# Performance work log

Measured on AMD Instinct MI355X. Metric: run time of the kernel, lower is better.

Reference implementation:

```python
import jax, jax.numpy as jnp
import numpy as np

RANK = 32
W0 = 30.0


def lip_linear(x, w, c, b=None):
    # LipschitzLinear: scale rows of w so row-wise L1 norm <= softplus(c)
    scale = jnp.minimum(jax.nn.softplus(c) / jnp.sum(jnp.abs(w), axis=-1), 1.0)
    y = x @ (w * scale[:, None]).T
    return y + b if b is not None else y


def setup_inputs() -> dict:
    key = jax.random.key(0)
    ks = jax.random.split(key, 20)
    d = {}
    d['coords'] = jax.random.normal(ks[0], (8, 32768, 3), dtype=jnp.float32)
    d['latents'] = jax.random.normal(ks[1], (8, 128), dtype=jnp.float32)
    d['nf_w_first'] = jax.random.normal(ks[2], (256, 3), dtype=jnp.float32)
    d['nf_b_first'] = jax.random.normal(ks[3], (256,), dtype=jnp.float32)
    d['nf_c_first'] = jax.random.uniform(ks[4], (1,), dtype=jnp.float32)
    d['nf_w_hid'] = jax.random.normal(ks[5], (3, 256, 256), dtype=jnp.float32)
    d['nf_b_hid'] = jax.random.normal(ks[6], (3, 256), dtype=jnp.float32)
    d['nf_c_hid'] = jax.random.uniform(ks[7], (3,), dtype=jnp.float32)
    d['nf_w_last'] = jax.random.normal(ks[8], (1, 256), dtype=jnp.float32)
    d['nf_b_last'] = jax.random.normal(ks[9], (1,), dtype=jnp.float32)
    d['nf_c_last'] = jax.random.uniform(ks[10], (1,), dtype=jnp.float32)
    d['Aw_first'] = jax.random.normal(ks[11], (96, 128), dtype=jnp.float32)
    d['Ac_first'] = jax.random.uniform(ks[12], (1,), dtype=jnp.float32)
    d['Aw_hid'] = jax.random.normal(ks[13], (3, 8192, 128), dtype=jnp.float32)
    d['Ac_hid'] = jax.random.uniform(ks[14], (3,), dtype=jnp.float32)
    d['Bw'] = jax.random.normal(ks[15], (4, 8192, 128), dtype=jnp.float32)
    d['Bc'] = jax.random.uniform(ks[16], (4,), dtype=jnp.float32)
    d['hbw'] = jax.random.normal(ks[17], (4, 256, 128), dtype=jnp.float32)
    d['hbc'] = jax.random.uniform(ks[18], (4,), dtype=jnp.float32)
    return d


def reference(coords, latents, nf_w_first, nf_b_first, nf_c_first, nf_w_hid, nf_b_hid, nf_c_hid,
              nf_w_last, nf_b_last, nf_c_last, Aw_first, Ac_first, Aw_hid, Ac_hid, Bw, Bc, hbw, hbc):
    T = latents.shape[0]
    # assemble per-layer params: (nf_w, nf_b, nf_c, A_w, A_c, B_w, B_c, hb_w, hb_c)
    layers = [(nf_w_first, nf_b_first, nf_c_first, Aw_first, Ac_first, Bw[0], Bc[0], hbw[0], hbc[0])]
    for j in range(nf_w_hid.shape[0]):
        layers.append((nf_w_hid[j], nf_b_hid[j], nf_c_hid[j], Aw_hid[j], Ac_hid[j],
                       Bw[j + 1], Bc[j + 1], hbw[j + 1], hbc[j + 1]))

    x = coords  # [T, N, d_in]
    for (w, b, c, aw, ac, bw, bc, hw, hc) in layers:
        d_out, d_in = w.shape
        A = lip_linear(latents, aw, ac).reshape(T, d_in, RANK)   # [T, d_in, r]
        B = lip_linear(latents, bw, bc).reshape(T, RANK, d_out)  # [T, r, d_out]
        bias = lip_linear(latents, hw, hc)                       # [T, d_out]
        base = lip_linear(x, w, c, b)                            # [T, N, d_out]
        mod = jnp.einsum('tnr,tro->tno', jnp.einsum('tni,tir->tnr', x, A), B)
        x = jnp.sin(W0 * (base + mod + bias[:, None, :]))
    return lip_linear(x, nf_w_last, nf_c_last, nf_b_last)  # [T, N, 1]
```

## Files before the change

kernel.cpp:

```cpp
#include <hip/hip_runtime.h>
#include <math.h>

#define W0F 30.0f
#define NPTS 32768

#define C_30_OVER_2PI 4.774648292756860070
#define C_2PI         6.283185307179586477

typedef double v4d __attribute__((ext_vector_type(4)));

#define OFF_M    0ull
#define SZ_M     2097152ull
#define OFF_CB   (OFF_M + SZ_M)
#define SZ_CB    8192ull
#define OFF_AF   (OFF_CB + SZ_CB)
#define SZ_AF    262144ull
#define OFF_BF   (OFF_AF + SZ_AF)
#define SZ_BF    262144ull
#define OFF_HB   (OFF_BF + SZ_BF)
#define SZ_HB    8192ull
#define OFF_NSC  (OFF_HB + SZ_HB)
#define SZ_NSC   2048ull
#define OFF_X    (OFF_NSC + SZ_NSC)
#define SZ_X     16777216ull

__global__ __launch_bounds__(256) void setup1(
    const float* __restrict__ latents,
    const float* __restrict__ AwF, const float* __restrict__ AcF,
    const float* __restrict__ AwH, const float* __restrict__ AcH,
    const float* __restrict__ Bw,  const float* __restrict__ Bc,
    const float* __restrict__ hbw, const float* __restrict__ hbc,
    const float* __restrict__ wF,  const float* __restrict__ cF,
    const float* __restrict__ wH,  const float* __restrict__ cH,
    const float* __restrict__ wL,  const float* __restrict__ cL,
    float* __restrict__ AF, float* __restrict__ BFo,
    float* __restrict__ HBo, float* __restrict__ NSC)
{
    __shared__ float lat[1024];
    int tid = threadIdx.x;
    for (int j = tid; j < 1024; j += 256) lat[j] = latents[j];
    __syncthreads();
    int g = blockIdx.x * 256 + tid;
    if (g < 58464) {
        const float* src; float c; float* dst; int stride;
        if (g < 96) {
            src = AwF + g * 128; c = AcF[0]; dst = AF + g; stride = 8192;
        } else if (g < 24672) {
            int q = g - 96; int l = 1 + q / 8192;
            src = AwH + (size_t)q * 128; c = AcH[l - 1];
            dst = AF + (size_t)l * 8 * 8192 + (q % 8192); stride = 8192;
        } else if (g < 57440) {
            int q = g - 24672; int l = q / 8192;
            src = Bw + (size_t)q * 128; c = Bc[l];
            dst = BFo + (size_t)l * 8 * 8192 + (q % 8192); stride = 8192;
        } else {
            int q = g - 57440; int l = q / 256;
            src = hbw + (size_t)q * 128; c = hbc[l];
            dst = HBo + l * 8 * 256 + (q % 256); stride = 256;
        }
        double l1 = 0.0;
        double acc[8] = {0,0,0,0,0,0,0,0};
        for (int kk = 0; kk < 32; ++kk) {
            float4 w4 = ((const float4*)src)[kk];
            l1 += fabs((double)w4.x) + fabs((double)w4.y)
                + fabs((double)w4.z) + fabs((double)w4.w);
            int k = kk * 4;
            #pragma unroll
            for (int t = 0; t < 8; ++t) {
                const float* lp = &lat[t * 128 + k];
                acc[t] = fma((double)w4.x, (double)lp[0], acc[t]);
                acc[t] = fma((double)w4.y, (double)lp[1], acc[t]);
                acc[t] = fma((double)w4.z, (double)lp[2], acc[t]);
                acc[t] = fma((double)w4.w, (double)lp[3], acc[t]);
            }
        }
        double s = fmin(log1p(exp((double)c)) / l1, 1.0);
        #pragma unroll
        for (int t = 0; t < 8; ++t) dst[(size_t)t * stride] = (float)(acc[t] * s);
    } else if (g < 59489) {
        int h = g - 58464;
        if (h < 256) {
            const float* src = wF + h * 3;
            double l1 = fabs((double)src[0]) + fabs((double)src[1]) + fabs((double)src[2]);
            NSC[h] = (float)fmin(log1p(exp((double)cF[0])) / l1, 1.0);
        } else if (h < 1024) {
            int q = h - 256; int l = 1 + q / 256;
            const float* src = wH + (size_t)q * 256;
            double l1 = 0.0;
            for (int kk = 0; kk < 64; ++kk) {
                float4 w4 = ((const float4*)src)[kk];
                l1 += fabs((double)w4.x) + fabs((double)w4.y)
                    + fabs((double)w4.z) + fabs((double)w4.w);
            }
            NSC[256 + q] = (float)fmin(log1p(exp((double)cH[l - 1])) / l1, 1.0);
        } else {
            double l1 = 0.0;
            for (int kk = 0; kk < 64; ++kk) {
                float4 w4 = ((const float4*)wL)[kk];
                l1 += fabs((double)w4.x) + fabs((double)w4.y)
                    + fabs((double)w4.z) + fabs((double)w4.w);
            }
            NSC[1024] = (float)fmin(log1p(exp((double)cL[0])) / l1, 1.0);
        }
    }
}

__global__ __launch_bounds__(256) void setup2(
    const float* __restrict__ wF, const float* __restrict__ bF,
    const float* __restrict__ wH, const float* __restrict__ bH,
    const float* __restrict__ AF, const float* __restrict__ BFi,
    const float* __restrict__ HBi, const float* __restrict__ NSC,
    float* __restrict__ Mb, float* __restrict__ CBb)
{
    int b = blockIdx.x; int t = b / 49; int rem = b % 49;
    int o = threadIdx.x;
    int l, i0, ni;
    if (rem == 0) { l = 0; i0 = 0; ni = 3; }
    else { l = 1 + (rem - 1) / 16; i0 = ((rem - 1) % 16) * 16; ni = 16; }
    size_t ltb = (size_t)(l * 8 + t);
    const float* af = AF + ltb * 8192;
    const float* bf = BFi + ltb * 8192;
    double sc = (double)NSC[l * 256 + o];
    float bcol[32];
    #pragma unroll
    for (int r = 0; r < 32; ++r) bcol[r] = bf[r * 256 + o];
    for (int ii = 0; ii < ni; ++ii) {
        int i = i0 + ii;
        float wv = (l == 0) ? wF[o * 3 + i] : wH[(size_t)((l - 1) * 256 + o) * 256 + i];
        double m = (double)wv * sc;
        #pragma unroll
        for (int r = 0; r < 32; ++r)
            m = fma((double)af[i * 32 + r], (double)bcol[r], m);
        Mb[ltb * 65536 + (size_t)i * 256 + o] = (float)m;
    }
    if (rem == 0 || ((rem - 1) % 16) == 0) {
        double bb = (l == 0) ? (double)bF[o] : (double)bH[(l - 1) * 256 + o];
        CBb[ltb * 256 + o] = (float)(bb + (double)HBi[ltb * 256 + o]);
    }
}

__device__ __forceinline__ float sin30(double z) {
    double u = z * C_30_OVER_2PI;
    double r = u - rint(u);
    return sinf((float)(r * C_2PI));
}

__global__ __launch_bounds__(256) void layer0_k(
    const float* __restrict__ coords, const float* __restrict__ Mb,
    const float* __restrict__ CBb, float* __restrict__ X, int tbase)
{
    __shared__ float Ms[3][256];
    __shared__ float cbs[256];
    int tid = threadIdx.x;
    int tl = blockIdx.x >> 10; int rb = blockIdx.x & 1023;
    int t = tbase + tl;
    const float* Mt = Mb + (size_t)t * 65536;
    Ms[0][tid] = Mt[tid]; Ms[1][tid] = Mt[256 + tid]; Ms[2][tid] = Mt[512 + tid];
    cbs[tid] = CBb[t * 256 + tid];
    __syncthreads();
    int r = rb * 32 + (tid >> 3); int lane8 = tid & 7;
    const float* cp = coords + ((size_t)t * NPTS + r) * 3;
    double c0 = (double)cp[0], c1 = (double)cp[1], c2 = (double)cp[2];
    float* xo = X + ((size_t)tl * NPTS + r) * 256;
#define L0E(col) sin30(fma(c2, (double)Ms[2][col], fma(c1, (double)Ms[1][col], \
                  fma(c0, (double)Ms[0][col], (double)cbs[col]))))
    #pragma unroll
    for (int j = 0; j < 8; ++j) {
        int col = 4 * lane8 + 32 * j;
        float4 v;
        v.x = L0E(col + 0);
        v.y = L0E(col + 1);
        v.z = L0E(col + 2);
        v.w = L0E(col + 3);
        *(float4*)(xo + col) = v;
    }
#undef L0E
}

__global__ __launch_bounds__(256, 2) void gemm_sin(
    float* __restrict__ X, const float* __restrict__ Mb,
    const float* __restrict__ CBb, int l, int tbase)
{
    __shared__ float As[16][72];
    __shared__ float Bs[16][264];
    __shared__ float cbs[256];
    int tid = threadIdx.x;
    int tl = blockIdx.x >> 9; int rb = blockIdx.x & 511;
    size_t ltb = (size_t)(l * 8 + tbase + tl);
    const float* Mt = Mb + ltb * 65536;
    float* Xt = X + ((size_t)tl * NPTS + rb * 64) * 256;
    cbs[tid] = CBb[ltb * 256 + tid];
    int wave = tid >> 6, lane = tid & 63;
    int q = lane >> 4, c16 = lane & 15;
    v4d zz = {0., 0., 0., 0.};
    v4d p1 = __builtin_amdgcn_mfma_f64_16x16x4f64((double)(1 << c16), 1.0, zz, 0, 0, 0);
    v4d p2 = __builtin_amdgcn_mfma_f64_16x16x4f64(1.0, (double)(1 << c16), zz, 0, 0, 0);
    int r0 = 61 - __builtin_clzll((unsigned long long)p1[0]);
    int r1 = 61 - __builtin_clzll((unsigned long long)p1[1]);
    int r2 = 61 - __builtin_clzll((unsigned long long)p1[2]);
    int r3 = 61 - __builtin_clzll((unsigned long long)p1[3]);
    int c0 = 61 - __builtin_clzll((unsigned long long)p2[0]);
    int c1 = 61 - __builtin_clzll((unsigned long long)p2[1]);
    int c2 = 61 - __builtin_clzll((unsigned long long)p2[2]);
    int c3 = 61 - __builtin_clzll((unsigned long long)p2[3]);
    int arow = tid >> 2;
    int ak4  = (tid & 3) * 4;
    int bch  = tid & 63;
    int br0  = tid >> 6;
    v4d acc0 = {0.,0.,0.,0.}, acc1 = {0.,0.,0.,0.}, acc2 = {0.,0.,0.,0.},
        acc3 = {0.,0.,0.,0.}, acc4 = {0.,0.,0.,0.}, acc5 = {0.,0.,0.,0.},
        acc6 = {0.,0.,0.,0.}, acc7 = {0.,0.,0.,0.}, acc8 = {0.,0.,0.,0.},
        acc9 = {0.,0.,0.,0.}, acc10 = {0.,0.,0.,0.}, acc11 = {0.,0.,0.,0.},
        acc12 = {0.,0.,0.,0.}, acc13 = {0.,0.,0.,0.}, acc14 = {0.,0.,0.,0.},
        acc15 = {0.,0.,0.,0.};
    for (int kb = 0; kb < 16; ++kb) {
        float4 a0 = *(const float4*)(Xt + (size_t)arow * 256 + kb * 16 + ak4);
        const float* Bg = Mt + (size_t)kb * 16 * 256 + bch * 4;
        float4 b0 = *(const float4*)(Bg + (br0 +  0) * 256);
        float4 b1 = *(const float4*)(Bg + (br0 +  4) * 256);
        float4 b2 = *(const float4*)(Bg + (br0 +  8) * 256);
        float4 b3 = *(const float4*)(Bg + (br0 + 12) * 256);
        __syncthreads();
        As[ak4+0][arow] = a0.x; As[ak4+1][arow] = a0.y;
        As[ak4+2][arow] = a0.z; As[ak4+3][arow] = a0.w;
        *(float4*)&Bs[br0 +  0][bch * 4] = b0;
        *(float4*)&Bs[br0 +  4][bch * 4] = b1;
        *(float4*)&Bs[br0 +  8][bch * 4] = b2;
        *(float4*)&Bs[br0 + 12][bch * 4] = b3;
        __syncthreads();
        #pragma unroll
        for (int k4 = 0; k4 < 4; ++k4) {
            int kk = k4 * 4 + q;
            double av = (double)As[kk][wave * 16 + c16];
#define TILE(n) { double bv = (double)Bs[kk][(n) * 16 + c16];                  \
                  acc##n = __builtin_amdgcn_mfma_f64_16x16x4f64(              \
                               av, bv, acc##n, 0, 0, 0); }
            TILE(0)  TILE(1)  TILE(2)  TILE(3)
            TILE(4)  TILE(5)  TILE(6)  TILE(7)
            TILE(8)  TILE(9)  TILE(10) TILE(11)
            TILE(12) TILE(13) TILE(14) TILE(15)
#undef TILE
        }
    }
    float* Xw = Xt + (size_t)(wave * 16) * 256;
#define EPT(n) {                                                               \
        int cb0 = (n) * 16;                                                    \
        Xw[r0 * 256 + cb0 + c0] = sin30(acc##n[0] + (double)cbs[cb0 + c0]);    \
        Xw[r1 * 256 + cb0 + c1] = sin30(acc##n[1] + (double)cbs[cb0 + c1]);    \
        Xw[r2 * 256 + cb0 + c2] = sin30(acc##n[2] + (double)cbs[cb0 + c2]);    \
        Xw[r3 * 256 + cb0 + c3] = sin30(acc##n[3] + (double)cbs[cb0 + c3]); }
    EPT(0)  EPT(1)  EPT(2)  EPT(3)
    EPT(4)  EPT(5)  EPT(6)  EPT(7)
    EPT(8)  EPT(9)  EPT(10) EPT(11)
    EPT(12) EPT(13) EPT(14) EPT(15)
#undef EPT
}

__global__ __launch_bounds__(256) void final_k(
    const float* __restrict__ X, const float* __restrict__ wl,
    const float* __restrict__ bl, const float* __restrict__ NSC,
    float* __restrict__ out, int tbase)
{
    int tid = threadIdx.x; int w = tid >> 6; int lane = tid & 63;
    size_t row = (size_t)blockIdx.x * 4 + w;
    double ls = (double)NSC[1024];
    float4 wv = ((const float4*)wl)[lane];
    float4 xv = *(const float4*)(X + row * 256 + lane * 4);
    double d = 0.0;
    d = fma((double)wv.x, (double)xv.x, d);
    d = fma((double)wv.y, (double)xv.y, d);
    d = fma((double)wv.z, (double)xv.z, d);
    d = fma((double)wv.w, (double)xv.w, d);
    d *= ls;
    #pragma unroll
    for (int off = 32; off > 0; off >>= 1) d += __shfl_down(d, off, 64);
    if (lane == 0) out[(size_t)tbase * NPTS + row] = (float)(d + (double)bl[0]);
}

extern "C" void kernel_launch(void* const* d_in, const int* in_sizes, int n_in,
                              void* d_out, int out_size, void* d_ws, size_t ws_size,
                              hipStream_t stream)
{
    const float* coords     = (const float*)d_in[0];
    const float* latents    = (const float*)d_in[1];
    const float* nf_w_first = (const float*)d_in[2];
    const float* nf_b_first = (const float*)d_in[3];
    const float* nf_c_first = (const float*)d_in[4];
    const float* nf_w_hid   = (const float*)d_in[5];
    const float* nf_b_hid   = (const float*)d_in[6];
    const float* nf_c_hid   = (const float*)d_in[7];
    const float* nf_w_last  = (const float*)d_in[8];
    const float* nf_b_last  = (const float*)d_in[9];
    const float* nf_c_last  = (const float*)d_in[10];
    const float* Aw_first   = (const float*)d_in[11];
    const float* Ac_first   = (const float*)d_in[12];
    const float* Aw_hid     = (const float*)d_in[13];
    const float* Ac_hid     = (const float*)d_in[14];
    const float* Bw         = (const float*)d_in[15];
    const float* Bc         = (const float*)d_in[16];
    const float* hbw        = (const float*)d_in[17];
    const float* hbc        = (const float*)d_in[18];

    float* ws  = (float*)d_ws;
    float* Mb  = ws + OFF_M;
    float* CBb = ws + OFF_CB;
    float* AF  = ws + OFF_AF;
    float* BFb = ws + OFF_BF;
    float* HBb = ws + OFF_HB;
    float* NSC = ws + OFF_NSC;
    float* X   = ws + OFF_X;
    float* out = (float*)d_out;

    setup1<<<233, 256, 0, stream>>>(latents, Aw_first, Ac_first, Aw_hid, Ac_hid,
                                    Bw, Bc, hbw, hbc,
                                    nf_w_first, nf_c_first, nf_w_hid, nf_c_hid,
                                    nf_w_last, nf_c_last,
                                    AF, BFb, HBb, NSC);
    setup2<<<392, 256, 0, stream>>>(nf_w_first, nf_b_first, nf_w_hid, nf_b_hid,
                                    AF, BFb, HBb, NSC, Mb, CBb);
    for (int tbase = 0; tbase < 8; tbase += 2) {
        layer0_k<<<2048, 256, 0, stream>>>(coords, Mb, CBb, X, tbase);
        for (int l = 1; l <= 3; ++l)
            gemm_sin<<<1024, 256, 0, stream>>>(X, Mb, CBb, l, tbase);
        final_k<<<16384, 256, 0, stream>>>(X, nf_w_last, nf_b_last, NSC, out, tbase);
    }
}
```

Before: 2.328 ms.

## Double-buffer shared-memory tiles in gemm_sin and raise occupancy hint

Splits the A and B shared-memory tiles into two buffers. Global loads for the next k-block are issued before the MFMA work on the current block, so load latency can overlap with compute and each iteration needs one barrier instead of two. Launch bounds move from 2 to 3 blocks per SM, which limits registers per thread. With 64 fp64 accumulator values plus the prefetch registers this risks spilling, and double buffering doubles LDS use.

```diff
diff --git a/kernel.cpp b/kernel.cpp
--- a/kernel.cpp
+++ b/kernel.cpp
@@ -177,12 +177,12 @@
 #undef L0E
 }
 
-__global__ __launch_bounds__(256, 2) void gemm_sin(
+__global__ __launch_bounds__(256, 3) void gemm_sin(
     float* __restrict__ X, const float* __restrict__ Mb,
     const float* __restrict__ CBb, int l, int tbase)
 {
-    __shared__ float As[16][72];
-    __shared__ float Bs[16][264];
+    __shared__ float As[2][16][72];
+    __shared__ float Bs[2][16][264];
     __shared__ float cbs[256];
     int tid = threadIdx.x;
     int tl = blockIdx.x >> 9; int rb = blockIdx.x & 511;
@@ -213,26 +213,38 @@
         acc9 = {0.,0.,0.,0.}, acc10 = {0.,0.,0.,0.}, acc11 = {0.,0.,0.,0.},
         acc12 = {0.,0.,0.,0.}, acc13 = {0.,0.,0.,0.}, acc14 = {0.,0.,0.,0.},
         acc15 = {0.,0.,0.,0.};
-    for (int kb = 0; kb < 16; ++kb) {
-        float4 a0 = *(const float4*)(Xt + (size_t)arow * 256 + kb * 16 + ak4);
-        const float* Bg = Mt + (size_t)kb * 16 * 256 + bch * 4;
+    {
+        float4 a0 = *(const float4*)(Xt + (size_t)arow * 256 + ak4);
+        const float* Bg = Mt + bch * 4;
         float4 b0 = *(const float4*)(Bg + (br0 +  0) * 256);
         float4 b1 = *(const float4*)(Bg + (br0 +  4) * 256);
         float4 b2 = *(const float4*)(Bg + (br0 +  8) * 256);
         float4 b3 = *(const float4*)(Bg + (br0 + 12) * 256);
-        __syncthreads();
-        As[ak4+0][arow] = a0.x; As[ak4+1][arow] = a0.y;
-        As[ak4+2][arow] = a0.z; As[ak4+3][arow] = a0.w;
-        *(float4*)&Bs[br0 +  0][bch * 4] = b0;
-        *(float4*)&Bs[br0 +  4][bch * 4] = b1;
-        *(float4*)&Bs[br0 +  8][bch * 4] = b2;
-        *(float4*)&Bs[br0 + 12][bch * 4] = b3;
-        __syncthreads();
+        As[0][ak4+0][arow] = a0.x; As[0][ak4+1][arow] = a0.y;
+        As[0][ak4+2][arow] = a0.z; As[0][ak4+3][arow] = a0.w;
+        *(float4*)&Bs[0][br0 +  0][bch * 4] = b0;
+        *(float4*)&Bs[0][br0 +  4][bch * 4] = b1;
+        *(float4*)&Bs[0][br0 +  8][bch * 4] = b2;
+        *(float4*)&Bs[0][br0 + 12][bch * 4] = b3;
+    }
+    __syncthreads();
+    #pragma unroll 2
+    for (int kb = 0; kb < 16; ++kb) {
+        int cur = kb & 1, nxt = cur ^ 1;
+        float4 a0, b0, b1, b2, b3;
+        if (kb < 15) {
+            a0 = *(const float4*)(Xt + (size_t)arow * 256 + (kb + 1) * 16 + ak4);
+            const float* Bg = Mt + (size_t)(kb + 1) * 16 * 256 + bch * 4;
+            b0 = *(const float4*)(Bg + (br0 +  0) * 256);
+            b1 = *(const float4*)(Bg + (br0 +  4) * 256);
+            b2 = *(const float4*)(Bg + (br0 +  8) * 256);
+            b3 = *(const float4*)(Bg + (br0 + 12) * 256);
+        }
         #pragma unroll
         for (int k4 = 0; k4 < 4; ++k4) {
             int kk = k4 * 4 + q;
-            double av = (double)As[kk][wave * 16 + c16];
-#define TILE(n) { double bv = (double)Bs[kk][(n) * 16 + c16];                  \
+            double av = (double)As[cur][kk][wave * 16 + c16];
+#define TILE(n) { double bv = (double)Bs[cur][kk][(n) * 16 + c16];             \
                   acc##n = __builtin_amdgcn_mfma_f64_16x16x4f64(              \
                                av, bv, acc##n, 0, 0, 0); }
             TILE(0)  TILE(1)  TILE(2)  TILE(3)
@@ -241,6 +253,15 @@
             TILE(12) TILE(13) TILE(14) TILE(15)
 #undef TILE
         }
+        if (kb < 15) {
+            As[nxt][ak4+0][arow] = a0.x; As[nxt][ak4+1][arow] = a0.y;
+            As[nxt][ak4+2][arow] = a0.z; As[nxt][ak4+3][arow] = a0.w;
+            *(float4*)&Bs[nxt][br0 +  0][bch * 4] = b0;
+            *(float4*)&Bs[nxt][br0 +  4][bch * 4] = b1;
+            *(float4*)&Bs[nxt][br0 +  8][bch * 4] = b2;
+            *(float4*)&Bs[nxt][br0 + 12][bch * 4] = b3;
+        }
+        __syncthreads();
     }
     float* Xw = Xt + (size_t)(wave * 16) * 256;
 #define EPT(n) {                                                               \
```

After: 2.186 ms. 1.07x faster.

## Split gemm_sin columns across blocks, read operands directly, ping-pong X buffers

Applied to the files above, without the earlier changes.

Each gemm_sin block now computes half of the 256 output columns for 64 rows, which doubles the grid and halves the accumulator count so that occupancy can rise to 4 blocks per SM. The LDS staging and the per-k-block __syncthreads are removed, and each lane loads its A and B scalars straight from global memory through the cache. Because two blocks now read the same rows in place, the layers ping-pong between two X buffers. This drops barrier and LDS overhead but issues many more uncoalesced scalar global loads and reads the A rows twice.

```diff
diff --git a/kernel.cpp b/kernel.cpp
--- a/kernel.cpp
+++ b/kernel.cpp
@@ -21,8 +21,9 @@
 #define SZ_HB    8192ull
 #define OFF_NSC  (OFF_HB + SZ_HB)
 #define SZ_NSC   2048ull
-#define OFF_X    (OFF_NSC + SZ_NSC)
+#define OFF_X0   (OFF_NSC + SZ_NSC)
 #define SZ_X     16777216ull
+#define OFF_X1   (OFF_X0 + SZ_X)
 
 __global__ __launch_bounds__(256) void setup1(
     const float* __restrict__ latents,
@@ -177,19 +178,21 @@
 #undef L0E
 }
 
-__global__ __launch_bounds__(256, 2) void gemm_sin(
-    float* __restrict__ X, const float* __restrict__ Mb,
-    const float* __restrict__ CBb, int l, int tbase)
-{
-    __shared__ float As[16][72];
-    __shared__ float Bs[16][264];
-    __shared__ float cbs[256];
+__global__ __launch_bounds__(256, 4) void gemm_sin(
+    const float* __restrict__ Xsrc, float* __restrict__ Xdst,
+    const float* __restrict__ Mb, const float* __restrict__ CBb,
+    int l, int tbase)
+{
     int tid = threadIdx.x;
-    int tl = blockIdx.x >> 9; int rb = blockIdx.x & 511;
+    int b = blockIdx.x;
+    int tl = b >> 10;
+    int rb = (b >> 1) & 511;
+    int ch = b & 1;
     size_t ltb = (size_t)(l * 8 + tbase + tl);
-    const float* Mt = Mb + ltb * 65536;
-    float* Xt = X + ((size_t)tl * NPTS + rb * 64) * 256;
-    cbs[tid] = CBb[ltb * 256 + tid];
+    const float* Mt  = Mb + ltb * 65536 + ch * 128;
+    const float* cbp = CBb + ltb * 256 + ch * 128;
+    const float* Xs = Xsrc + ((size_t)tl * NPTS + rb * 64) * 256;
+    float*       Xd = Xdst + ((size_t)tl * NPTS + rb * 64) * 256 + ch * 128;
     int wave = tid >> 6, lane = tid & 63;
     int q = lane >> 4, c16 = lane & 15;
     v4d zz = {0., 0., 0., 0.};
@@ -203,56 +206,31 @@
     int c1 = 61 - __builtin_clzll((unsigned long long)p2[1]);
     int c2 = 61 - __builtin_clzll((unsigned long long)p2[2]);
     int c3 = 61 - __builtin_clzll((unsigned long long)p2[3]);
-    int arow = tid >> 2;
-    int ak4  = (tid & 3) * 4;
-    int bch  = tid & 63;
-    int br0  = tid >> 6;
+    const float* ap = Xs + (size_t)(wave * 16 + c16) * 256 + q;
+    const float* bp = Mt + (size_t)q * 256 + c16;
     v4d acc0 = {0.,0.,0.,0.}, acc1 = {0.,0.,0.,0.}, acc2 = {0.,0.,0.,0.},
         acc3 = {0.,0.,0.,0.}, acc4 = {0.,0.,0.,0.}, acc5 = {0.,0.,0.,0.},
-        acc6 = {0.,0.,0.,0.}, acc7 = {0.,0.,0.,0.}, acc8 = {0.,0.,0.,0.},
-        acc9 = {0.,0.,0.,0.}, acc10 = {0.,0.,0.,0.}, acc11 = {0.,0.,0.,0.},
-        acc12 = {0.,0.,0.,0.}, acc13 = {0.,0.,0.,0.}, acc14 = {0.,0.,0.,0.},
-        acc15 = {0.,0.,0.,0.};
-    for (int kb = 0; kb < 16; ++kb) {
-        float4 a0 = *(const float4*)(Xt + (size_t)arow * 256 + kb * 16 + ak4);
-        const float* Bg = Mt + (size_t)kb * 16 * 256 + bch * 4;
-        float4 b0 = *(const float4*)(Bg + (br0 +  0) * 256);
-        float4 b1 = *(const float4*)(Bg + (br0 +  4) * 256);
-        float4 b2 = *(const float4*)(Bg + (br0 +  8) * 256);
-        float4 b3 = *(const float4*)(Bg + (br0 + 12) * 256);
-        __syncthreads();
-        As[ak4+0][arow] = a0.x; As[ak4+1][arow] = a0.y;
-        As[ak4+2][arow] = a0.z; As[ak4+3][arow] = a0.w;
-        *(float4*)&Bs[br0 +  0][bch * 4] = b0;
-        *(float4*)&Bs[br0 +  4][bch * 4] = b1;
-        *(float4*)&Bs[br0 +  8][bch * 4] = b2;
-        *(float4*)&Bs[br0 + 12][bch * 4] = b3;
-        __syncthreads();
-        #pragma unroll
-        for (int k4 = 0; k4 < 4; ++k4) {
-            int kk = k4 * 4 + q;
-            double av = (double)As[kk][wave * 16 + c16];
-#define TILE(n) { double bv = (double)Bs[kk][(n) * 16 + c16];                  \
+        acc6 = {0.,0.,0.,0.}, acc7 = {0.,0.,0.,0.};
+    #pragma unroll 4
+    for (int s = 0; s < 64; ++s) {
+        double av = (double)ap[4 * s];
+        const float* bb = bp + (size_t)s * 1024;
+#define TILE(n) { double bv = (double)bb[(n) * 16];                            \
                   acc##n = __builtin_amdgcn_mfma_f64_16x16x4f64(              \
                                av, bv, acc##n, 0, 0, 0); }
-            TILE(0)  TILE(1)  TILE(2)  TILE(3)
-            TILE(4)  TILE(5)  TILE(6)  TILE(7)
-            TILE(8)  TILE(9)  TILE(10) TILE(11)
-            TILE(12) TILE(13) TILE(14) TILE(15)
+        TILE(0) TILE(1) TILE(2) TILE(3)
+        TILE(4) TILE(5) TILE(6) TILE(7)
 #undef TILE
-        }
-    }
-    float* Xw = Xt + (size_t)(wave * 16) * 256;
+    }
+    float* Xw = Xd + (size_t)(wave * 16) * 256;
 #define EPT(n) {                                                               \
         int cb0 = (n) * 16;                                                    \
-        Xw[r0 * 256 + cb0 + c0] = sin30(acc##n[0] + (double)cbs[cb0 + c0]);    \
-        Xw[r1 * 256 + cb0 + c1] = sin30(acc##n[1] + (double)cbs[cb0 + c1]);    \
-        Xw[r2 * 256 + cb0 + c2] = sin30(acc##n[2] + (double)cbs[cb0 + c2]);    \
-        Xw[r3 * 256 + cb0 + c3] = sin30(acc##n[3] + (double)cbs[cb0 + c3]); }
-    EPT(0)  EPT(1)  EPT(2)  EPT(3)
-    EPT(4)  EPT(5)  EPT(6)  EPT(7)
-    EPT(8)  EPT(9)  EPT(10) EPT(11)
-    EPT(12) EPT(13) EPT(14) EPT(15)
+        Xw[r0 * 256 + cb0 + c0] = sin30(acc##n[0] + (double)cbp[cb0 + c0]);    \
+        Xw[r1 * 256 + cb0 + c1] = sin30(acc##n[1] + (double)cbp[cb0 + c1]);    \
+        Xw[r2 * 256 + cb0 + c2] = sin30(acc##n[2] + (double)cbp[cb0 + c2]);    \
+        Xw[r3 * 256 + cb0 + c3] = sin30(acc##n[3] + (double)cbp[cb0 + c3]); }
+    EPT(0) EPT(1) EPT(2) EPT(3)
+    EPT(4) EPT(5) EPT(6) EPT(7)
 #undef EPT
 }
 
@@ -308,7 +286,8 @@
     float* BFb = ws + OFF_BF;
     float* HBb = ws + OFF_HB;
     float* NSC = ws + OFF_NSC;
-    float* X   = ws + OFF_X;
+    float* X0  = ws + OFF_X0;
+    float* X1  = ws + OFF_X1;
     float* out = (float*)d_out;
 
     setup1<<<233, 256, 0, stream>>>(latents, Aw_first, Ac_first, Aw_hid, Ac_hid,
@@ -319,9 +298,10 @@
     setup2<<<392, 256, 0, stream>>>(nf_w_first, nf_b_first, nf_w_hid, nf_b_hid,
                                     AF, BFb, HBb, NSC, Mb, CBb);
     for (int tbase = 0; tbase < 8; tbase += 2) {
-        layer0_k<<<2048, 256, 0, stream>>>(coords, Mb, CBb, X, tbase);
-        for (int l = 1; l <= 3; ++l)
-            gemm_sin<<<1024, 256, 0, stream>>>(X, Mb, CBb, l, tbase);
-        final_k<<<16384, 256, 0, stream>>>(X, nf_w_last, nf_b_last, NSC, out, tbase);
-    }
-}
+        layer0_k<<<2048, 256, 0, stream>>>(coords, Mb, CBb, X0, tbase);
+        gemm_sin<<<2048, 256, 0, stream>>>(X0, X1, Mb, CBb, 1, tbase);
+        gemm_sin<<<2048, 256, 0, stream>>>(X1, X0, Mb, CBb, 2, tbase);
+        gemm_sin<<<2048, 256, 0, stream>>>(X0, X1, Mb, CBb, 3, tbase);
+        final_k<<<16384, 256, 0, stream>>>(X1, nf_w_last, nf_b_last, NSC, out, tbase);
+    }
+}
```

Result: slower. 2.757 ms (+18.4%).
